# Kernel optimization log

Measured on AMD Instinct MI355X. Metric: run time of the kernel, lower is better.

The kernel has to match this reference:

```python
import jax, jax.numpy as jnp
import numpy as np

C = 256
HEADS = 4
ATT = C // HEADS
GROUPS = 32
EPS = 1e-6


def group_norm(x, gamma, beta):
    # x: [b, c, h, w]
    b, c, h, w = x.shape
    xg = x.reshape(b, GROUPS, c // GROUPS, h, w)
    mu = jnp.mean(xg, axis=(2, 3, 4), keepdims=True)
    var = jnp.var(xg, axis=(2, 3, 4), keepdims=True)
    xg = (xg - mu) * jax.lax.rsqrt(var + EPS)
    x = xg.reshape(b, c, h, w)
    return x * gamma[None, :, None, None] + beta[None, :, None, None]


def conv1x1(x, w, b):
    # w: [c_out, c_in], x: [b, c_in, h, w]
    return jnp.einsum('oc,bchw->bohw', w, x) + b[None, :, None, None]


def setup_inputs() -> dict:
    key = jax.random.key(0)
    ks = jax.random.split(key, 8)
    b, h, w = 2, 64, 64
    x = jax.random.normal(ks[0], (b, C, h, w), dtype=jnp.float32)
    y = jax.random.normal(ks[1], (b, C, h, w), dtype=jnp.float32)
    s = 1.0 / np.sqrt(C)
    return {
        'x': x,
        'y': y,
        'g1': jnp.ones((C,), jnp.float32),
        'b1': jnp.zeros((C,), jnp.float32),
        'g2': jnp.ones((C,), jnp.float32),
        'b2': jnp.zeros((C,), jnp.float32),
        'wq': jax.random.normal(ks[2], (C, C), jnp.float32) * s,
        'bq': jnp.zeros((C,), jnp.float32),
        'wk': jax.random.normal(ks[3], (C, C), jnp.float32) * s,
        'bk': jnp.zeros((C,), jnp.float32),
        'wv': jax.random.normal(ks[4], (C, C), jnp.float32) * s,
        'bv': jnp.zeros((C,), jnp.float32),
        'wo': jax.random.normal(ks[5], (C, C), jnp.float32) * s,
        'bo': jnp.zeros((C,), jnp.float32),
    }


def reference(x, y, g1, b1, g2, b2, wq, bq, wk, bk, wv, bv, wo, bo):
    b, c, h, w = x.shape
    s = h * w
    h_ = group_norm(x, g1, b1)
    yn = group_norm(y, g2, b2)
    q = conv1x1(yn, wq, bq)
    k = conv1x1(h_, wk, bk)
    v = conv1x1(h_, wv, bv)
    # [b, c, h, w] -> [b, heads, att, s] -> [b, heads, s, att]
    def split_heads(t):
        return t.reshape(b, HEADS, ATT, s).transpose(0, 1, 3, 2)
    q = split_heads(q) * (ATT ** -0.5)
    k = split_heads(k)
    v = split_heads(v)
    scores = jnp.einsum('bnsd,bntd->bnst', q, k)        # [b, heads, s, s]
    attn = jax.nn.softmax(scores, axis=-1)
    out = jnp.einsum('bnst,bntd->bnsd', attn, v)        # [b, heads, s, att]
    # [b, heads, s, att] -> [b, s, heads, att] -> [b, h, w, c] -> [b, c, h, w]
    out = out.transpose(0, 2, 1, 3).reshape(b, h, w, c).transpose(0, 3, 1, 2)
    out = conv1x1(out, wo, bo)
    return x + out
```

## Files before the change

### kernel.cpp

```cpp
#include <hip/hip_runtime.h>

typedef __bf16 bf16_t;
typedef bf16_t bf16x8 __attribute__((ext_vector_type(8)));
typedef float f32x4 __attribute__((ext_vector_type(4)));

#define MFMA16(a,b,c) __builtin_amdgcn_mfma_f32_16x16x32_bf16((a),(b),(c),0,0,0)

#define GLOAD_LDS16(gsrc, ldst) \
  __builtin_amdgcn_global_load_lds((const __attribute__((address_space(1))) unsigned int*)(gsrc), \
                                   (__attribute__((address_space(3))) unsigned int*)(ldst), 16, 0, 0)

__device__ __forceinline__ unsigned short f2bf(float f){
  unsigned int u = __builtin_bit_cast(unsigned int, f);
  u = (u + 0x7FFFu + ((u >> 16) & 1u)) >> 16;
  return (unsigned short)u;
}
__device__ __forceinline__ float bf2f(unsigned short u){
  return __builtin_bit_cast(float, (unsigned int)u << 16);
}
__device__ __forceinline__ ushort4 pk4(f32x4 v){
  union { __bf16 b[4]; ushort4 u; } r;
  r.b[0]=(__bf16)v[0]; r.b[1]=(__bf16)v[1]; r.b[2]=(__bf16)v[2]; r.b[3]=(__bf16)v[3];
  return r.u;
}
__device__ __forceinline__ unsigned cvtpk(float lo, float hi){
  unsigned r; asm("v_cvt_pk_bf16_f32 %0, %1, %2" : "=v"(r) : "v"(lo), "v"(hi)); return r;
}
__device__ __forceinline__ float max3f(float a, float b, float c){
  float r; asm("v_max3_f32 %0, %1, %2, %3" : "=v"(r) : "v"(a), "v"(b), "v"(c)); return r;
}

__device__ __forceinline__ int KI(int d){
  int gi = (d >> 2) & 15;
  int pos = (gi & 8) | ((gi & 3) << 1) | ((gi >> 2) & 1);
  return (d & ~63) | (pos << 2);
}

__device__ __forceinline__ int BL256(int r, int c){
  return ((r >> 4) << 12) + (((c >> 5)) << 9) + ((r & 15) << 5)
       + (((c & 15) >> 2) << 3) + (((c >> 4) & 1) << 2) + (c & 3);
}

constexpr int BN = 2;
constexpr int CC = 256;
constexpr int S  = 4096;
constexpr int HH = 4;
constexpr int DD = 64;

constexpr size_t OFF_WQ = 0;
constexpr size_t OFF_WK = 65536;
constexpr size_t OFF_WV = 131072;
constexpr size_t OFF_WO = 196608;
constexpr size_t OFF_NY = 262144;
constexpr size_t OFF_NX = OFF_NY + (size_t)BN*S*CC;
constexpr size_t OFF_Q  = OFF_NX + (size_t)BN*S*CC;
constexpr size_t OFF_K  = OFF_Q  + (size_t)BN*S*CC;
constexpr size_t OFF_V  = OFF_K  + (size_t)BN*S*CC;
constexpr size_t OFF_AO = OFF_V  + (size_t)BN*S*CC;
__device__ __forceinline__ unsigned short* pacc_base(unsigned short* ws, int ch){
  return ws + (ch == 0 ? OFF_NY : (ch == 1 ? OFF_NX : OFF_AO));
}

__global__ __launch_bounds__(256) void prep_k(const float* __restrict__ x, const float* __restrict__ y,
    const float* __restrict__ g1, const float* __restrict__ b1,
    const float* __restrict__ g2, const float* __restrict__ b2,
    const float* __restrict__ wq, const float* __restrict__ wk,
    const float* __restrict__ wv, const float* __restrict__ wo,
    unsigned short* __restrict__ ws)
{
  __shared__ float red[8];
  __shared__ float mv[2];
  const int tid = threadIdx.x;
  const int bid = blockIdx.x;

  if (bid >= 128){
    const int idx = (bid - 128)*256 + tid;
    const int m = idx >> 14;
    const int off = (idx & 16383) << 2;
    const float* src = (m==0) ? wq : (m==1) ? wk : (m==2) ? wv : wo;
    float4 v = *(const float4*)(src + off);
    ushort4 r; r.x=f2bf(v.x); r.y=f2bf(v.y); r.z=f2bf(v.z); r.w=f2bf(v.w);
    const int o = off >> 8, c = off & 255;
    *(ushort4*)(ws + (size_t)m*65536 + BL256(o, c)) = r;
    return;
  }

  const int tsel = bid >> 6;
  const int rem  = bid & 63;
  const int b = rem >> 5, g = rem & 31;
  const float* in = (tsel ? y : x) + ((size_t)b*CC + g*8)*S;
  unsigned short* outp = ws + (tsel ? OFF_NY : OFF_NX) + (size_t)b*S*CC;
  const int j = g & 3;
  const int gk = (g >> 2) * 512;
  const int posA = (j & 1)*16 + (j >> 1)*4;
  const int posB = posA + 8;
  const float* gamma = (tsel ? g2 : g1) + g*8;
  const float* beta  = (tsel ? b2 : b1) + g*8;

  float s = 0.f, ss = 0.f;
  #pragma unroll
  for (int ci = 0; ci < 8; ci++){
    const float4* row = (const float4*)(in + (size_t)ci*S);
    #pragma unroll
    for (int i = 0; i < 4; i++){
      float4 v = row[tid + i*256];
      s  += v.x + v.y + v.z + v.w;
      ss += v.x*v.x + v.y*v.y + v.z*v.z + v.w*v.w;
    }
  }
  #pragma unroll
  for (int off = 1; off < 64; off <<= 1){
    s  += __shfl_xor(s,  off);
    ss += __shfl_xor(ss, off);
  }
  const int wave = tid >> 6, lane = tid & 63;
  if (lane == 0){ red[wave] = s; red[4+wave] = ss; }
  __syncthreads();
  if (tid == 0){
    float S1 = red[0]+red[1]+red[2]+red[3];
    float S2 = red[4]+red[5]+red[6]+red[7];
    const float invn = 1.0f/32768.0f;
    float mean = S1*invn;
    float var  = S2*invn - mean*mean;
    mv[0] = mean; mv[1] = rsqrtf(var + 1e-6f);
  }
  __syncthreads();
  const float mean = mv[0], rstd = mv[1];
  float sc[8], sh[8];
  #pragma unroll
  for (int ci = 0; ci < 8; ci++){ sc[ci] = rstd*gamma[ci]; sh[ci] = beta[ci] - mean*sc[ci]; }
  for (int i = 0; i < 16; i++){
    const int p = tid + i*256;
    const int base = ((p >> 4) << 12) + gk + ((p & 15) << 5);
    ushort4 a0, a1;
    a0.x = f2bf(in[0*S+p]*sc[0]+sh[0]);
    a0.y = f2bf(in[1*S+p]*sc[1]+sh[1]);
    a0.z = f2bf(in[2*S+p]*sc[2]+sh[2]);
    a0.w = f2bf(in[3*S+p]*sc[3]+sh[3]);
    a1.x = f2bf(in[4*S+p]*sc[4]+sh[4]);
    a1.y = f2bf(in[5*S+p]*sc[5]+sh[5]);
    a1.z = f2bf(in[6*S+p]*sc[6]+sh[6]);
    a1.w = f2bf(in[7*S+p]*sc[7]+sh[7]);
    *(ushort4*)(outp + base + posA) = a0;
    *(ushort4*)(outp + base + posB) = a1;
  }
}

__global__ __launch_bounds__(256, 3) void qkv_gemm(unsigned short* __restrict__ ws,
    const float* __restrict__ bq, const float* __restrict__ bk, const float* __restrict__ bv)
{
  __shared__ unsigned short stg[8192];
  const int tid = threadIdx.x;
  const int lane = tid & 63, wave = tid >> 6;
  const int lq = lane & 15, lg = lane >> 4;
  const int lofs = lq*32 + lg*8;
  const int bid = blockIdx.x;

  if (bid < 512){
    const int inst2 = bid >> 7;
    const int which = inst2 >> 1;
    const int b = inst2 & 1;
    const int tile = bid & 127;
    const int mtile = tile & 3;
    const int ntile = tile >> 2;
    const int mbase = mtile*64 + (wave>>1)*32;
    const int nbase = ntile*128 + (wave&1)*64;
    const unsigned short* Amat = ws + (which==0 ? OFF_WQ : OFF_WK);
    const unsigned short* Bmat = ws + (which==0 ? OFF_NY : OFF_NX) + (size_t)b*S*CC;

    f32x4 acc[2][4];
    #pragma unroll
    for (int i = 0; i < 2; i++)
      #pragma unroll
      for (int j = 0; j < 4; j++)
        acc[i][j] = (f32x4){0.f,0.f,0.f,0.f};

    const unsigned short* Arow = Amat + (size_t)mbase*CC + lofs;
    const unsigned short* Brow = Bmat + (size_t)nbase*CC + lofs;
    for (int ks = 0; ks < CC; ks += 32) {
      bf16x8 af[2], bfr[4];
      #pragma unroll
      for (int mt = 0; mt < 2; mt++)
        af[mt] = *(const bf16x8*)(Arow + mt*16*CC + ks*16);
      #pragma unroll
      for (int nt = 0; nt < 4; nt++)
        bfr[nt] = *(const bf16x8*)(Brow + nt*16*CC + ks*16);
      #pragma unroll
      for (int mt = 0; mt < 2; mt++)
        #pragma unroll
        for (int nt = 0; nt < 4; nt++)
          acc[mt][nt] = MFMA16(af[mt], bfr[nt], acc[mt][nt]);
    }

    const float* bias = (which==0) ? bq : bk;
    const float scl = (which==0) ? 0.125f*1.44269504089f : 1.0f;
    unsigned short* Outp = ws + (which==0 ? OFF_Q : OFF_K) + (size_t)b*HH*S*DD;
    #pragma unroll
    for (int mt = 0; mt < 2; mt++){
      const int o = mbase + mt*16 + lg*4;
      const float4 bb = *(const float4*)(bias + o);
      const int db = KI(o & 63);
      #pragma unroll
      for (int nt = 0; nt < 4; nt++){
        const int lp = (wave&1)*64 + nt*16 + lq;
        f32x4 v = acc[mt][nt];
        ushort4 r;
        r.x = f2bf((v[0]+bb.x)*scl); r.y = f2bf((v[1]+bb.y)*scl);
        r.z = f2bf((v[2]+bb.z)*scl); r.w = f2bf((v[3]+bb.w)*scl);
        *(ushort4*)(stg + lp*64 + (db ^ ((lp & 7) << 3))) = r;
      }
    }
    __syncthreads();
    #pragma unroll
    for (int k = 0; k < 4; k++){
      const int c = tid + k*256;
      const int row = c >> 3, gl = (c & 7) << 3;
      uint4 v = *(const uint4*)(stg + row*64 + (gl ^ ((row & 7) << 3)));
      *(uint4*)(Outp + ((size_t)mtile*S + ntile*128 + row)*DD + gl) = v;
    }
  } else {
    const int r0 = bid - 512;
    const int b = r0 >> 7;
    const int tile = r0 & 127;
    const int mtile = tile >> 2;
    const int ntile = tile & 3;
    const int mbase = mtile*128 + (wave>>1)*64;
    const int nbase = ntile*64 + (wave&1)*32;
    const unsigned short* Amat = ws + OFF_NX + (size_t)b*S*CC;
    const unsigned short* Bmat = ws + OFF_WV;

    f32x4 acc[4][2];
    #pragma unroll
    for (int i = 0; i < 4; i++)
      #pragma unroll
      for (int j = 0; j < 2; j++)
        acc[i][j] = (f32x4){0.f,0.f,0.f,0.f};

    const unsigned short* Arow = Amat + (size_t)mbase*CC + lofs;
    const unsigned short* Brow = Bmat + (size_t)nbase*CC + lofs;
    for (int ks = 0; ks < CC; ks += 32) {
      bf16x8 af[4], bfr[2];
      #pragma unroll
      for (int mt = 0; mt < 4; mt++)
        af[mt] = *(const bf16x8*)(Arow + mt*16*CC + ks*16);
      #pragma unroll
      for (int nt = 0; nt < 2; nt++)
        bfr[nt] = *(const bf16x8*)(Brow + nt*16*CC + ks*16);
      #pragma unroll
      for (int mt = 0; mt < 4; mt++)
        #pragma unroll
        for (int nt = 0; nt < 2; nt++)
          acc[mt][nt] = MFMA16(af[mt], bfr[nt], acc[mt][nt]);
    }

    unsigned short* Outp = ws + OFF_V + (size_t)b*CC*S;
    #pragma unroll
    for (int nt = 0; nt < 2; nt++){
      const int o = nbase + nt*16 + lq;
      const int ro = o - ntile*64;
      const float bb = bv[o];
      #pragma unroll
      for (int mt = 0; mt < 4; mt++){
        const int lp = (wave>>1)*64 + mt*16 + lg*4;
        f32x4 v = acc[mt][nt];
        ushort4 r;
        r.x = f2bf(v[0]+bb); r.y = f2bf(v[1]+bb);
        r.z = f2bf(v[2]+bb); r.w = f2bf(v[3]+bb);
        *(ushort4*)(stg + ro*128 + (KI(lp) ^ ((ro & 7) << 3))) = r;
      }
    }
    __syncthreads();
    #pragma unroll
    for (int k = 0; k < 4; k++){
      const int c = tid + k*256;
      const int row = c >> 4, gl = (c & 15) << 3;
      uint4 v = *(const uint4*)(stg + row*128 + (gl ^ ((row & 7) << 3)));
      *(uint4*)(Outp + (size_t)(ntile*64 + row)*S + mtile*128 + gl) = v;
    }
  }
}

__global__ __launch_bounds__(256, 3) void attn_k(unsigned short* __restrict__ ws)
{
  __shared__ __align__(1024) char lds[32768];
  const int tid = threadIdx.x;
  const int lane = tid & 63, wave = tid >> 6;
  const int lq = lane & 15, lg = lane >> 4;
  const int rsw = (lq & 7) << 4;
  const int bid = blockIdx.x;
  const int bh = bid & 7;
  const int rest = bid >> 3;
  const int qblk = rest & 31;
  const int ch = rest >> 5;
  const int tBeg = ch*1344 + (ch ? 64 : 0);
  const int tEnd = tBeg + 1344 + (ch ? 0 : 64);
  const unsigned short* Qp = ws + OFF_Q + (size_t)bh*S*DD;
  const unsigned short* Kp = ws + OFF_K + (size_t)bh*S*DD;
  const int b = bh >> 2, h = bh & 3;
  const unsigned short* Vp = ws + OFF_V + ((size_t)b*CC + h*DD)*S;
  const int qbw = qblk*128 + wave*32;

  bf16x8 qf[2][2];
  #pragma unroll
  for (int f = 0; f < 2; f++)
    #pragma unroll
    for (int hh = 0; hh < 2; hh++)
      qf[f][hh] = *(const bf16x8*)(Qp + (size_t)(qbw + f*16 + lq)*DD + hh*32 + lg*8);

  bf16x8 ones;
  #pragma unroll
  for (int i = 0; i < 8; i++) ones[i] = (__bf16)1.0f;

  const int csel = ((lane & 7) ^ ((lane >> 3) & 7)) * 8;
  const int srow = wave*16 + (lane >> 3);
  const int kofs0 = lq*128 + ((lg*16) ^ rsw);
  const int kofs1 = kofs0 ^ 64;

  f32x4 acc[4][2];
  #pragma unroll
  for (int i = 0; i < 4; i++)
    #pragma unroll
    for (int f = 0; f < 2; f++)
      acc[i][f] = (f32x4){0.f,0.f,0.f,0.f};
  f32x4 accL[2] = {(f32x4){0.f,0.f,0.f,0.f}, (f32x4){0.f,0.f,0.f,0.f}};
  float mr[2] = {-1e30f, -1e30f};

  #pragma unroll
  for (int j = 0; j < 2; j++){
    const int row = srow + j*8;
    GLOAD_LDS16(Kp + (size_t)(tBeg + row)*DD + csel, lds + wave*2048 + j*1024);
    GLOAD_LDS16(Vp + (size_t)row*S + tBeg + csel,    lds + 16384 + wave*2048 + j*1024);
  }
  __syncthreads();

  int cur = 0;
  for (int t0 = tBeg; t0 < tEnd; t0 += 64){
    const char* kb = lds + cur*8192;
    const char* vb = lds + 16384 + cur*8192;
    if (t0 + 64 < tEnd){
      char* kn = lds + (cur^1)*8192;
      char* vn = lds + 16384 + (cur^1)*8192;
      #pragma unroll
      for (int j = 0; j < 2; j++){
        const int row = srow + j*8;
        GLOAD_LDS16(Kp + (size_t)(t0 + 64 + row)*DD + csel, kn + wave*2048 + j*1024);
        GLOAD_LDS16(Vp + (size_t)row*S + (t0 + 64) + csel,  vn + wave*2048 + j*1024);
      }
    }
    bf16x8 kf[4][2];
    #pragma unroll
    for (int mt = 0; mt < 4; mt++){
      kf[mt][0] = *(const bf16x8*)(kb + mt*2048 + kofs0);
      kf[mt][1] = *(const bf16x8*)(kb + mt*2048 + kofs1);
    }
    f32x4 st[2][4];
    #pragma unroll
    for (int f = 0; f < 2; f++)
      #pragma unroll
      for (int mt = 0; mt < 4; mt++){
        f32x4 z = (f32x4){0.f,0.f,0.f,0.f};
        z = MFMA16(kf[mt][0], qf[f][0], z);
        z = MFMA16(kf[mt][1], qf[f][1], z);
        st[f][mt] = z;
      }
    bf16x8 vf[4][2];
    #pragma unroll
    for (int dt = 0; dt < 4; dt++){
      vf[dt][0] = *(const bf16x8*)(vb + dt*2048 + kofs0);
      vf[dt][1] = *(const bf16x8*)(vb + dt*2048 + kofs1);
    }
    float tmv[2];
    #pragma unroll
    for (int f = 0; f < 2; f++){
      float m1 = max3f(st[f][0][0], st[f][0][1], st[f][0][2]);
      float m2 = max3f(st[f][0][3], st[f][1][0], st[f][1][1]);
      float m3 = max3f(st[f][1][2], st[f][1][3], st[f][2][0]);
      float m4 = max3f(st[f][2][1], st[f][2][2], st[f][2][3]);
      float m5 = max3f(st[f][3][0], st[f][3][1], st[f][3][2]);
      float tm = fmaxf(fmaxf(max3f(m1, m2, m3), fmaxf(m4, m5)), st[f][3][3]);
      tm = fmaxf(tm, __shfl_xor(tm, 16));
      tm = fmaxf(tm, __shfl_xor(tm, 32));
      tmv[f] = tm;
    }
    if (!__all((tmv[0] <= mr[0] + 8.f) && (tmv[1] <= mr[1] + 8.f))){
      #pragma unroll
      for (int f = 0; f < 2; f++){
        const float mnew = fmaxf(mr[f], tmv[f]);
        const float c = __builtin_amdgcn_exp2f(mr[f] - mnew);
        #pragma unroll
        for (int dt = 0; dt < 4; dt++)
          #pragma unroll
          for (int r = 0; r < 4; r++)
            acc[dt][f][r] *= c;
        #pragma unroll
        for (int r = 0; r < 4; r++) accL[f][r] *= c;
        mr[f] = mnew;
      }
    }
    union PU { bf16x8 v; unsigned u[4]; } p0[2], p1[2];
    #pragma unroll
    for (int f = 0; f < 2; f++){
      #pragma unroll
      for (int mt = 0; mt < 4; mt++){
        float e0 = __builtin_amdgcn_exp2f(st[f][mt][0] - mr[f]);
        float e1 = __builtin_amdgcn_exp2f(st[f][mt][1] - mr[f]);
        float e2 = __builtin_amdgcn_exp2f(st[f][mt][2] - mr[f]);
        float e3 = __builtin_amdgcn_exp2f(st[f][mt][3] - mr[f]);
        if (mt < 2){ p0[f].u[mt*2] = cvtpk(e0, e1); p0[f].u[mt*2+1] = cvtpk(e2, e3); }
        else       { p1[f].u[(mt-2)*2] = cvtpk(e0, e1); p1[f].u[(mt-2)*2+1] = cvtpk(e2, e3); }
      }
    }
    #pragma unroll
    for (int dt = 0; dt < 4; dt++)
      #pragma unroll
      for (int f = 0; f < 2; f++){
        f32x4 a = acc[dt][f];
        a = MFMA16(vf[dt][0], p0[f].v, a);
        a = MFMA16(vf[dt][1], p1[f].v, a);
        acc[dt][f] = a;
      }
    #pragma unroll
    for (int f = 0; f < 2; f++){
      accL[f] = MFMA16(ones, p0[f].v, accL[f]);
      accL[f] = MFMA16(ones, p1[f].v, accL[f]);
    }
    __syncthreads();
    cur ^= 1;
  }

  unsigned short* PA = pacc_base(ws, ch) + (size_t)bh*S*DD;
  float* ML = (float*)(ws + OFF_Q) + ((size_t)ch*8 + bh)*S*2;
  #pragma unroll
  for (int f = 0; f < 2; f++){
    const int q = qbw + f*16 + lq;
    #pragma unroll
    for (int dt = 0; dt < 4; dt++)
      *(ushort4*)(PA + (size_t)q*DD + dt*16 + lg*4) = pk4(acc[dt][f]);
    if (lg == 0){
      ML[(size_t)q*2]   = mr[f];
      ML[(size_t)q*2+1] = accL[f][0];
    }
  }
}

__global__ __launch_bounds__(256, 2) void outproj_k(unsigned short* __restrict__ ws,
    const float* __restrict__ bo, const float* __restrict__ x, float* __restrict__ out)
{
  __shared__ unsigned short ldsA[8192];
  __shared__ float wtab[32][4][3];
  const int tid = threadIdx.x;
  const int lane = tid & 63, wave = tid >> 6;
  const int lq = lane & 15, lg = lane >> 4;
  const int lofs = lq*32 + lg*8;
  const int bid = blockIdx.x;
  const int b = bid >> 8;
  const int r0 = bid & 255;
  const int mtile = r0 >> 1;
  const int ntile = r0 & 1;
  const int qg = mtile*32;

  if (tid < 128){
    const int q = tid >> 2, h = tid & 3;
    const float* MLb = (const float*)(ws + OFF_Q);
    float m[3], l[3];
    #pragma unroll
    for (int c = 0; c < 3; c++){
      const float* p = MLb + (((size_t)c*8 + b*4 + h)*S + (qg + q))*2;
      m[c] = p[0]; l[c] = p[1];
    }
    const float M = fmaxf(m[0], fmaxf(m[1], m[2]));
    const float w0 = __builtin_amdgcn_exp2f(m[0] - M);
    const float w1 = __builtin_amdgcn_exp2f(m[1] - M);
    const float w2 = __builtin_amdgcn_exp2f(m[2] - M);
    const float inv = 1.0f / (w0*l[0] + w1*l[1] + w2*l[2]);
    wtab[q][h][0] = w0*inv; wtab[q][h][1] = w1*inv; wtab[q][h][2] = w2*inv;
  }
  __syncthreads();

  #pragma unroll
  for (int it = 0; it < 8; it++){
    const int w = it*256 + tid;
    const int q = w >> 6, cq = w & 63;
    const int h = cq >> 4, d = (cq & 15)*4;
    const size_t po = ((size_t)(b*4 + h)*S + (qg + q))*DD + d;
    const ushort4 a0 = *(const ushort4*)(ws + OFF_NY + po);
    const ushort4 a1 = *(const ushort4*)(ws + OFF_NX + po);
    const ushort4 a2 = *(const ushort4*)(ws + OFF_AO + po);
    const float w0 = wtab[q][h][0], w1 = wtab[q][h][1], w2 = wtab[q][h][2];
    f32x4 v;
    v[0] = bf2f(a0.x)*w0 + bf2f(a1.x)*w1 + bf2f(a2.x)*w2;
    v[1] = bf2f(a0.y)*w0 + bf2f(a1.y)*w1 + bf2f(a2.y)*w2;
    v[2] = bf2f(a0.z)*w0 + bf2f(a1.z)*w1 + bf2f(a2.z)*w2;
    v[3] = bf2f(a0.w)*w0 + bf2f(a1.w)*w1 + bf2f(a2.w)*w2;
    *(ushort4*)(ldsA + BL256(q, cq*4)) = pk4(v);
  }
  __syncthreads();

  const int mf = wave & 1;
  const int nb = ntile*128 + (wave >> 1)*64;
  f32x4 acc[4];
  #pragma unroll
  for (int i = 0; i < 4; i++) acc[i] = (f32x4){0.f,0.f,0.f,0.f};
  const unsigned short* Arow = ldsA + mf*16*CC + lofs;
  const unsigned short* Brow = ws + OFF_WO + (size_t)nb*CC + lofs;
  for (int ks = 0; ks < CC; ks += 32) {
    bf16x8 af = *(const bf16x8*)(Arow + ks*16);
    bf16x8 bfr[4];
    #pragma unroll
    for (int nt = 0; nt < 4; nt++)
      bfr[nt] = *(const bf16x8*)(Brow + nt*16*CC + ks*16);
    #pragma unroll
    for (int nt = 0; nt < 4; nt++)
      acc[nt] = MFMA16(af, bfr[nt], acc[nt]);
  }
  #pragma unroll
  for (int nt = 0; nt < 4; nt++){
    const int o = nb + nt*16 + lq;
    const float bb = bo[o];
    const int p = qg + mf*16 + lg*4;
    const size_t idx = ((size_t)b*CC + o)*S + p;
    const float4 xr = *(const float4*)(x + idx);
    f32x4 v = acc[nt];
    float4 r; r.x = v[0]+bb+xr.x; r.y = v[1]+bb+xr.y; r.z = v[2]+bb+xr.z; r.w = v[3]+bb+xr.w;
    *(float4*)(out + idx) = r;
  }
}

extern "C" void kernel_launch(void* const* d_in, const int* in_sizes, int n_in,
                              void* d_out, int out_size, void* d_ws, size_t ws_size,
                              hipStream_t stream) {
  const float* x  = (const float*)d_in[0];
  const float* y  = (const float*)d_in[1];
  const float* g1 = (const float*)d_in[2];
  const float* b1 = (const float*)d_in[3];
  const float* g2 = (const float*)d_in[4];
  const float* b2 = (const float*)d_in[5];
  const float* wq = (const float*)d_in[6];
  const float* bq = (const float*)d_in[7];
  const float* wk = (const float*)d_in[8];
  const float* bk = (const float*)d_in[9];
  const float* wv = (const float*)d_in[10];
  const float* bv = (const float*)d_in[11];
  const float* wo = (const float*)d_in[12];
  const float* bo = (const float*)d_in[13];
  float* out = (float*)d_out;
  unsigned short* ws16 = (unsigned short*)d_ws;

  prep_k   <<<384, 256, 0, stream>>>(x, y, g1, b1, g2, b2, wq, wk, wv, wo, ws16);
  qkv_gemm <<<768, 256, 0, stream>>>(ws16, bq, bk, bv);
  attn_k   <<<768, 256, 0, stream>>>(ws16);
  outproj_k<<<512, 256, 0, stream>>>(ws16, bo, x, out);
}
```

Before: 104.8 us.

## Split group-norm prep into separate stats and apply kernels with vectorized loads

The fused prep kernel, which ran only 128 blocks for the group-norm work, becomes two kernels. A stats kernel uses 256 blocks, each reducing half a group, and writes partial sums to scratch space in the AO workspace region. An apply kernel uses 256 norm blocks plus the weight-conversion blocks, combines the partials and normalizes with float4 loads instead of scalar loads. This raises parallelism and load width for a memory-bound step, at the cost of one extra launch and reading the inputs twice from memory or L2.

Result: faster. 88.85 us (-15.2%).

```diff
diff --git a/kernel.cpp b/kernel.cpp
--- a/kernel.cpp
+++ b/kernel.cpp
@@ -61,20 +61,57 @@
   return ws + (ch == 0 ? OFF_NY : (ch == 1 ? OFF_NX : OFF_AO));
 }
 
-__global__ __launch_bounds__(256) void prep_k(const float* __restrict__ x, const float* __restrict__ y,
+__global__ __launch_bounds__(256) void stats_k(const float* __restrict__ x, const float* __restrict__ y,
+    unsigned short* __restrict__ ws)
+{
+  __shared__ float red[8];
+  const int tid = threadIdx.x;
+  const int bid = blockIdx.x;
+  const int hh = bid & 1;
+  const int g = (bid >> 1) & 31;
+  const int b = (bid >> 6) & 1;
+  const int tsel = bid >> 7;
+  const float* in = (tsel ? y : x) + ((size_t)b*CC + g*8)*S + hh*2048;
+
+  float s = 0.f, ss = 0.f;
+  #pragma unroll
+  for (int ci = 0; ci < 8; ci++){
+    const float4* row = (const float4*)(in + (size_t)ci*S);
+    #pragma unroll
+    for (int i = 0; i < 2; i++){
+      float4 v = row[tid + i*256];
+      s  += v.x + v.y + v.z + v.w;
+      ss += v.x*v.x + v.y*v.y + v.z*v.z + v.w*v.w;
+    }
+  }
+  #pragma unroll
+  for (int off = 1; off < 64; off <<= 1){
+    s  += __shfl_xor(s,  off);
+    ss += __shfl_xor(ss, off);
+  }
+  const int wave = tid >> 6, lane = tid & 63;
+  if (lane == 0){ red[wave] = s; red[4+wave] = ss; }
+  __syncthreads();
+  if (tid == 0){
+    float* stats = (float*)(ws + OFF_AO);
+    const int unit = (tsel*2 + b)*32 + g;
+    stats[unit*4 + hh*2]     = red[0]+red[1]+red[2]+red[3];
+    stats[unit*4 + hh*2 + 1] = red[4]+red[5]+red[6]+red[7];
+  }
+}
+
+__global__ __launch_bounds__(256) void apply_k(const float* __restrict__ x, const float* __restrict__ y,
     const float* __restrict__ g1, const float* __restrict__ b1,
     const float* __restrict__ g2, const float* __restrict__ b2,
     const float* __restrict__ wq, const float* __restrict__ wk,
     const float* __restrict__ wv, const float* __restrict__ wo,
     unsigned short* __restrict__ ws)
 {
-  __shared__ float red[8];
-  __shared__ float mv[2];
   const int tid = threadIdx.x;
   const int bid = blockIdx.x;
 
-  if (bid >= 128){
-    const int idx = (bid - 128)*256 + tid;
+  if (bid >= 256){
+    const int idx = (bid - 256)*256 + tid;
     const int m = idx >> 14;
     const int off = (idx & 16383) << 2;
     const float* src = (m==0) ? wq : (m==1) ? wk : (m==2) ? wv : wo;
@@ -85,64 +122,56 @@
     return;
   }
 
-  const int tsel = bid >> 6;
-  const int rem  = bid & 63;
-  const int b = rem >> 5, g = rem & 31;
+  const int hh = bid & 1;
+  const int g = (bid >> 1) & 31;
+  const int b = (bid >> 6) & 1;
+  const int tsel = bid >> 7;
   const float* in = (tsel ? y : x) + ((size_t)b*CC + g*8)*S;
   unsigned short* outp = ws + (tsel ? OFF_NY : OFF_NX) + (size_t)b*S*CC;
+  const int gk = (g >> 2) * 512;
   const int j = g & 3;
-  const int gk = (g >> 2) * 512;
   const int posA = (j & 1)*16 + (j >> 1)*4;
   const int posB = posA + 8;
   const float* gamma = (tsel ? g2 : g1) + g*8;
   const float* beta  = (tsel ? b2 : b1) + g*8;
 
-  float s = 0.f, ss = 0.f;
-  #pragma unroll
-  for (int ci = 0; ci < 8; ci++){
-    const float4* row = (const float4*)(in + (size_t)ci*S);
-    #pragma unroll
-    for (int i = 0; i < 4; i++){
-      float4 v = row[tid + i*256];
-      s  += v.x + v.y + v.z + v.w;
-      ss += v.x*v.x + v.y*v.y + v.z*v.z + v.w*v.w;
-    }
-  }
-  #pragma unroll
-  for (int off = 1; off < 64; off <<= 1){
-    s  += __shfl_xor(s,  off);
-    ss += __shfl_xor(ss, off);
-  }
-  const int wave = tid >> 6, lane = tid & 63;
-  if (lane == 0){ red[wave] = s; red[4+wave] = ss; }
-  __syncthreads();
-  if (tid == 0){
-    float S1 = red[0]+red[1]+red[2]+red[3];
-    float S2 = red[4]+red[5]+red[6]+red[7];
-    const float invn = 1.0f/32768.0f;
-    float mean = S1*invn;
-    float var  = S2*invn - mean*mean;
-    mv[0] = mean; mv[1] = rsqrtf(var + 1e-6f);
-  }
-  __syncthreads();
-  const float mean = mv[0], rstd = mv[1];
+  const float* stats = (const float*)(ws + OFF_AO);
+  const int unit = (tsel*2 + b)*32 + g;
+  const float s  = stats[unit*4] + stats[unit*4 + 2];
+  const float ssum = stats[unit*4 + 1] + stats[unit*4 + 3];
+  const float invn = 1.0f/32768.0f;
+  const float mean = s*invn;
+  const float var  = ssum*invn - mean*mean;
+  const float rstd = rsqrtf(var + 1e-6f);
   float sc[8], sh[8];
   #pragma unroll
   for (int ci = 0; ci < 8; ci++){ sc[ci] = rstd*gamma[ci]; sh[ci] = beta[ci] - mean*sc[ci]; }
-  for (int i = 0; i < 16; i++){
-    const int p = tid + i*256;
-    const int base = ((p >> 4) << 12) + gk + ((p & 15) << 5);
-    ushort4 a0, a1;
-    a0.x = f2bf(in[0*S+p]*sc[0]+sh[0]);
-    a0.y = f2bf(in[1*S+p]*sc[1]+sh[1]);
-    a0.z = f2bf(in[2*S+p]*sc[2]+sh[2]);
-    a0.w = f2bf(in[3*S+p]*sc[3]+sh[3]);
-    a1.x = f2bf(in[4*S+p]*sc[4]+sh[4]);
-    a1.y = f2bf(in[5*S+p]*sc[5]+sh[5]);
-    a1.z = f2bf(in[6*S+p]*sc[6]+sh[6]);
-    a1.w = f2bf(in[7*S+p]*sc[7]+sh[7]);
-    *(ushort4*)(outp + base + posA) = a0;
-    *(ushort4*)(outp + base + posB) = a1;
+
+  #pragma unroll
+  for (int i = 0; i < 2; i++){
+    float4 v[8];
+    #pragma unroll
+    for (int ci = 0; ci < 8; ci++)
+      v[ci] = ((const float4*)(in + (size_t)ci*S + hh*2048))[tid + i*256];
+    const int p0 = hh*2048 + 4*(tid + i*256);
+    const int base = ((p0 >> 4) << 12) + gk;
+    #pragma unroll
+    for (int jj = 0; jj < 4; jj++){
+      const int p = p0 + jj;
+      const int rowo = base + ((p & 15) << 5);
+      float e0 = ((const float*)&v[0])[jj]*sc[0]+sh[0];
+      float e1 = ((const float*)&v[1])[jj]*sc[1]+sh[1];
+      float e2 = ((const float*)&v[2])[jj]*sc[2]+sh[2];
+      float e3 = ((const float*)&v[3])[jj]*sc[3]+sh[3];
+      float e4 = ((const float*)&v[4])[jj]*sc[4]+sh[4];
+      float e5 = ((const float*)&v[5])[jj]*sc[5]+sh[5];
+      float e6 = ((const float*)&v[6])[jj]*sc[6]+sh[6];
+      float e7 = ((const float*)&v[7])[jj]*sc[7]+sh[7];
+      ushort4 a0; a0.x=f2bf(e0); a0.y=f2bf(e1); a0.z=f2bf(e2); a0.w=f2bf(e3);
+      ushort4 a1; a1.x=f2bf(e4); a1.y=f2bf(e5); a1.z=f2bf(e6); a1.w=f2bf(e7);
+      *(ushort4*)(outp + rowo + posA) = a0;
+      *(ushort4*)(outp + rowo + posB) = a1;
+    }
   }
 }
 
@@ -546,7 +575,8 @@
   float* out = (float*)d_out;
   unsigned short* ws16 = (unsigned short*)d_ws;
 
-  prep_k   <<<384, 256, 0, stream>>>(x, y, g1, b1, g2, b2, wq, wk, wv, wo, ws16);
+  stats_k  <<<256, 256, 0, stream>>>(x, y, ws16);
+  apply_k  <<<512, 256, 0, stream>>>(x, y, g1, b1, g2, b2, wq, wk, wv, wo, ws16);
   qkv_gemm <<<768, 256, 0, stream>>>(ws16, bq, bk, bv);
   attn_k   <<<768, 256, 0, stream>>>(ws16);
   outproj_k<<<512, 256, 0, stream>>>(ws16, bo, x, out);
```
